# Optimization experiments

Hardware: AMD Instinct MI355X
Metric: run time of the kernel (lower is better)

Reference implementation:

```python
import jax, jax.numpy as jnp
import numpy as np

BOTTLENECK_DIM = 128
TOP_K = 8
SCALE = 1.0 / np.sqrt(BOTTLENECK_DIM)
EPS = 1e-10


def setup_inputs() -> dict:
    key = jax.random.key(0)
    k1, k2, k3, k4 = jax.random.split(key, 4)
    query = jax.random.normal(k1, (4, 4096, 128), dtype=jnp.float32)
    keys = jax.random.normal(k2, (4096, 128), dtype=jnp.float32)
    values = jax.random.normal(k3, (4096, 1024), dtype=jnp.float32)
    reliability = jax.random.uniform(k4, (4096,), dtype=jnp.float32)
    return {"query": query, "keys": keys, "values": values, "reliability": reliability}


def reference(query, keys, values, reliability):
    # Routing: [b, s, num_slots] scores with log-reliability bias, take top-k slots.
    router_scores = jnp.einsum("bsd,nd->bsn", query, keys) + jnp.log(reliability + EPS)
    _, top_indices = jax.lax.top_k(router_scores, TOP_K)  # [b, s, k]

    # Gather per-token slot keys/values: [b, s, k, d] and [b, s, k, h]
    selected_keys = keys[top_indices]
    selected_values = values[top_indices]

    # Small-k attention over gathered slots.
    attn_scores = jnp.einsum("bsd,bskd->bsk", query, selected_keys) * SCALE
    attn_weights = jax.nn.softmax(attn_scores, axis=-1)  # [b, s, k]
    output = jnp.einsum("bsk,bskh->bsh", attn_weights, selected_values)
    return output, attn_weights
```

## Files before the change

kernel.cpp:

```cpp
#include <hip/hip_runtime.h>
#include <hip/hip_fp16.h>
#include <math.h>

#define NSLOTS 4096
#define DIM    128
#define HDIM   1024
#define NTOK   16384
#define SCALE  0.08838834764831845f
#define REPS   1e-10f

typedef __attribute__((ext_vector_type(8))) short bf16x8;
typedef __attribute__((ext_vector_type(4))) float f32x4;

typedef __attribute__((address_space(1))) const void* as1cv;
typedef __attribute__((address_space(3))) void* as3v;

__device__ __forceinline__ float pack_score(float biased, unsigned inv_idx) {
    return __uint_as_float((__float_as_uint(biased) & 0xFFFFF000u) | inv_idx);
}
#define PACK_NEG_INF __uint_as_float(0xFF7FF000u)

__device__ __forceinline__ void ins_packed(float (&r)[8], float x) {
    #pragma unroll
    for (int i = 0; i < 7; ++i) r[i] = __builtin_amdgcn_fmed3f(r[i], x, r[i + 1]);
    r[7] = fmaxf(r[7], x);
}

__device__ __forceinline__ void merge_out16(float (&r)[8], int kseg, float* outS) {
    float hv = r[7];
    #pragma unroll
    for (int rnd = 0; rnd < 16; ++rnd) {
        float bv = hv;
        bv = fmaxf(bv, __shfl_xor(bv, 16, 64));
        bv = fmaxf(bv, __shfl_xor(bv, 32, 64));
        if ((rnd >> 2) == kseg) outS[rnd] = bv;
        if (hv == bv) {
            #pragma unroll
            for (int m2 = 7; m2 > 0; --m2) r[m2] = r[m2 - 1];
            r[0] = PACK_NEG_INF;
            hv = r[7];
        }
    }
}

__device__ __forceinline__ ushort f2bf(float f) {
    unsigned u = __float_as_uint(f);
    return (ushort)((u + 0x7fffu + ((u >> 16) & 1u)) >> 16);
}
#define QB_N  524288
#define KBP_N 65536
#define LR_N  4096
#define VH_N  524288
__global__ void prep_kernel(const float* __restrict__ q, const float* __restrict__ k,
                            const float* __restrict__ rel, const float* __restrict__ v,
                            ushort* __restrict__ qb, ushort* __restrict__ kbp,
                            float* __restrict__ lr, ushort* __restrict__ vh) {
    int gid = blockIdx.x * 256 + threadIdx.x;
    if (gid < QB_N) {
        float4 vv = ((const float4*)q)[gid];
        ushort4 o; o.x = f2bf(vv.x); o.y = f2bf(vv.y); o.z = f2bf(vv.z); o.w = f2bf(vv.w);
        ((ushort4*)qb)[gid] = o;
    } else if (gid < QB_N + KBP_N) {
        int C = gid - QB_N;
        int l = C & 63, kc = (C >> 6) & 3, t16 = C >> 8;
        int slot = t16 * 16 + (l & 15);
        int doff = kc * 32 + (l >> 4) * 8;
        const float4* src = (const float4*)(k + (size_t)slot * DIM + doff);
        float4 v0 = src[0], v1 = src[1];
        union { ushort u[8]; uint4 v; } o;
        o.u[0] = f2bf(v0.x); o.u[1] = f2bf(v0.y); o.u[2] = f2bf(v0.z); o.u[3] = f2bf(v0.w);
        o.u[4] = f2bf(v1.x); o.u[5] = f2bf(v1.y); o.u[6] = f2bf(v1.z); o.u[7] = f2bf(v1.w);
        ((uint4*)kbp)[C] = o.v;
    } else if (gid < QB_N + KBP_N + LR_N) {
        int g = gid - QB_N - KBP_N;
        lr[g] = logf(rel[g] + REPS);
    } else if (gid < QB_N + KBP_N + LR_N + VH_N) {
        int g = gid - QB_N - KBP_N - LR_N;
        const float4* src = (const float4*)v + (size_t)g * 2;
        float4 a = src[0], b = src[1];
        union { _Float16 h[8]; uint4 u; } o;
        o.h[0] = (_Float16)a.x; o.h[1] = (_Float16)a.y;
        o.h[2] = (_Float16)a.z; o.h[3] = (_Float16)a.w;
        o.h[4] = (_Float16)b.x; o.h[5] = (_Float16)b.y;
        o.h[6] = (_Float16)b.z; o.h[7] = (_Float16)b.w;
        ((uint4*)vh)[g] = o.u;
    }
}

__launch_bounds__(256, 4)
__global__ void route_kernel(const ushort* __restrict__ qb,
                             const ushort* __restrict__ kbp,
                             const float*  __restrict__ lr,
                             int* __restrict__ cand) {
    __shared__ ushort ktile[4][2][4 * 512];
    __shared__ float  qS[32][4][16];
    const int tid  = threadIdx.x;
    const int lane = tid & 63;
    const int w    = tid >> 6;
    const int m    = lane & 15;
    const int kseg = lane >> 4;
    const int tokbase = blockIdx.x * 32;

    bf16x8 bF0[4], bF1[4];
    const ushort* q0 = qb + (size_t)(tokbase + m) * DIM + kseg * 8;
    const ushort* q1 = qb + (size_t)(tokbase + 16 + m) * DIM + kseg * 8;
    #pragma unroll
    for (int kc = 0; kc < 4; ++kc) {
        bF0[kc] = *(const bf16x8*)(q0 + kc * 32);
        bF1[kc] = *(const bf16x8*)(q1 + kc * 32);
    }

    float R0[8], R1[8];
    #pragma unroll
    for (int i = 0; i < 8; ++i) { R0[i] = PACK_NEG_INF; R1[i] = PACK_NEG_INF; }

    auto issue = [&](int t, int buf) {
        const ushort* gt = kbp + ((size_t)((w * 64 + t) * 256 + lane)) * 8;
        ushort* lb = &ktile[w][buf][0];
        #pragma unroll
        for (int i = 0; i < 4; ++i) {
            __builtin_amdgcn_global_load_lds((as1cv)(gt + i * 512),
                                             (as3v)(lb + i * 512 + lane * 8), 16, 0, 0);
        }
    };

    issue(0, 0);
    issue(1, 1);

    for (int t = 0; t < 64; ++t) {
        const int cur = t & 1;
        if (t < 63) {
            asm volatile("s_waitcnt vmcnt(4)" ::: "memory");
        } else {
            asm volatile("s_waitcnt vmcnt(0)" ::: "memory");
        }
        const ushort* kt = &ktile[w][cur][0];
        bf16x8 aF[4];
        #pragma unroll
        for (int kc = 0; kc < 4; ++kc)
            aF[kc] = *(const bf16x8*)(kt + kc * 512 + lane * 8);
        asm volatile("s_waitcnt lgkmcnt(0)" ::: "memory");
        if (t < 62) issue(t + 2, cur);

        f32x4 acc0 = {0.f, 0.f, 0.f, 0.f};
        f32x4 acc1 = {0.f, 0.f, 0.f, 0.f};
        #pragma unroll
        for (int kc = 0; kc < 4; ++kc) {
            acc0 = __builtin_amdgcn_mfma_f32_16x16x32_bf16(aF[kc], bF0[kc], acc0, 0, 0, 0);
            acc1 = __builtin_amdgcn_mfma_f32_16x16x32_bf16(aF[kc], bF1[kc], acc1, 0, 0, 0);
        }
        const int base = w * 1024 + t * 16;
        float4 lrv = ((const float4*)lr)[(base >> 2) + kseg];
        unsigned invb = 4095u - (unsigned)(base + kseg * 4);
        ins_packed(R0, pack_score(acc0[0] + lrv.x, invb));
        ins_packed(R0, pack_score(acc0[1] + lrv.y, invb - 1));
        ins_packed(R0, pack_score(acc0[2] + lrv.z, invb - 2));
        ins_packed(R0, pack_score(acc0[3] + lrv.w, invb - 3));
        ins_packed(R1, pack_score(acc1[0] + lrv.x, invb));
        ins_packed(R1, pack_score(acc1[1] + lrv.y, invb - 1));
        ins_packed(R1, pack_score(acc1[2] + lrv.z, invb - 2));
        ins_packed(R1, pack_score(acc1[3] + lrv.w, invb - 3));
    }

    merge_out16(R0, kseg, &qS[m][w][0]);
    merge_out16(R1, kseg, &qS[m + 16][w][0]);
    __syncthreads();

    if (tid < 32) {
        const int token = tokbase + tid;
        int p[4] = {0, 0, 0, 0};
        #pragma unroll
        for (int c = 0; c < 16; ++c) {
            float bv = -INFINITY; int bq = 0;
            #pragma unroll
            for (int j = 0; j < 4; ++j) {
                float v = (p[j] < 16) ? qS[tid][j][p[j]] : -INFINITY;
                if (v > bv) { bv = v; bq = j; }
            }
            cand[(size_t)token * 16 + c] = 4095 - (int)(__float_as_uint(bv) & 0xFFFu);
            ++p[bq];
        }
    }
}

__device__ __forceinline__ float2 h2f2(unsigned u) {
    return __half22float2(*reinterpret_cast<const __half2*>(&u));
}
__launch_bounds__(512, 4)
__global__ void rescue_gather_kernel(const float* __restrict__ query,
                                     const float* __restrict__ keys,
                                     const float* __restrict__ lr,
                                     const int*   __restrict__ cand,
                                     const ushort* __restrict__ vh,
                                     float* __restrict__ out,
                                     float* __restrict__ wout) {
    __shared__ float4 pbuf[4][4][64];
    const int tid  = threadIdx.x;
    const int wv   = tid >> 6;
    const int tw   = wv >> 1;
    const int par  = wv & 1;
    const int lane = tid & 63;
    const int token = blockIdx.x * 4 + tw;
    const int c  = lane >> 2;
    const int qp = lane & 3;

    int ci = cand[(size_t)token * 16 + c];
    const float4* q4 = (const float4*)(query + (size_t)token * DIM) + qp * 8;
    const float4* k4 = (const float4*)(keys  + (size_t)ci    * DIM) + qp * 8;
    float sum = 0.f;
    #pragma unroll
    for (int i = 0; i < 8; ++i) {
        float4 a = q4[i], b = k4[i];
        sum = fmaf(a.x, b.x, sum); sum = fmaf(a.y, b.y, sum);
        sum = fmaf(a.z, b.z, sum); sum = fmaf(a.w, b.w, sum);
    }
    sum += __shfl_xor(sum, 1, 4);
    sum += __shfl_xor(sum, 2, 4);
    float raw = sum;
    float s   = sum + lr[ci];

    #pragma unroll
    for (int k = 2; k <= 16; k <<= 1) {
        #pragma unroll
        for (int j = k >> 1; j >= 1; j >>= 1) {
            int off = j << 2;
            float s2 = __shfl_xor(s,   off, 64);
            float r2 = __shfl_xor(raw, off, 64);
            int   i2 = __shfl_xor(ci,  off, 64);
            bool mineFirst = (s > s2) || (s == s2 && ci < i2);
            bool lower = (c & j) == 0;
            bool asc   = (c & k) == 0;
            bool keep  = (lower == asc) ? mineFirst : !mineFirst;
            if (!keep) { s = s2; raw = r2; ci = i2; }
        }
    }
    float rsel[8]; int isel[8];
    #pragma unroll
    for (int r = 0; r < 8; ++r) {
        rsel[r] = __shfl(raw, r * 4, 64);
        isel[r] = __shfl(ci,  r * 4, 64);
    }

    float mx = -INFINITY;
    #pragma unroll
    for (int k = 0; k < 8; ++k) { rsel[k] *= SCALE; mx = fmaxf(mx, rsel[k]); }
    float e[8]; float ssum = 0.f;
    #pragma unroll
    for (int k = 0; k < 8; ++k) { e[k] = expf(rsel[k] - mx); ssum += e[k]; }
    float inv = 1.0f / ssum;
    float wk[8];
    #pragma unroll
    for (int k = 0; k < 8; ++k) wk[k] = e[k] * inv;

    if (par == 0 && lane == 0) {
        #pragma unroll
        for (int k = 0; k < 8; ++k) wout[(size_t)token * 8 + k] = wk[k];
    }

    float oA[8], oB[8];
    #pragma unroll
    for (int i = 0; i < 8; ++i) { oA[i] = 0.f; oB[i] = 0.f; }
    #pragma unroll
    for (int kk = 0; kk < 4; ++kk) {
        const int k = par * 4 + kk;
        const uint4* vr = (const uint4*)vh + (size_t)isel[k] * 128;
        float wkk = wk[k];
        uint4 va = vr[lane];
        uint4 vb = vr[lane + 64];
        float2 f;
        f = h2f2(va.x); oA[0] = fmaf(wkk, f.x, oA[0]); oA[1] = fmaf(wkk, f.y, oA[1]);
        f = h2f2(va.y); oA[2] = fmaf(wkk, f.x, oA[2]); oA[3] = fmaf(wkk, f.y, oA[3]);
        f = h2f2(va.z); oA[4] = fmaf(wkk, f.x, oA[4]); oA[5] = fmaf(wkk, f.y, oA[5]);
        f = h2f2(va.w); oA[6] = fmaf(wkk, f.x, oA[6]); oA[7] = fmaf(wkk, f.y, oA[7]);
        f = h2f2(vb.x); oB[0] = fmaf(wkk, f.x, oB[0]); oB[1] = fmaf(wkk, f.y, oB[1]);
        f = h2f2(vb.y); oB[2] = fmaf(wkk, f.x, oB[2]); oB[3] = fmaf(wkk, f.y, oB[3]);
        f = h2f2(vb.z); oB[4] = fmaf(wkk, f.x, oB[4]); oB[5] = fmaf(wkk, f.y, oB[5]);
        f = h2f2(vb.w); oB[6] = fmaf(wkk, f.x, oB[6]); oB[7] = fmaf(wkk, f.y, oB[7]);
    }

    if (par) {
        pbuf[tw][0][lane] = make_float4(oA[0], oA[1], oA[2], oA[3]);
        pbuf[tw][1][lane] = make_float4(oA[4], oA[5], oA[6], oA[7]);
        pbuf[tw][2][lane] = make_float4(oB[0], oB[1], oB[2], oB[3]);
        pbuf[tw][3][lane] = make_float4(oB[4], oB[5], oB[6], oB[7]);
    }
    __syncthreads();
    if (!par) {
        float4 pA0 = pbuf[tw][0][lane], pA1 = pbuf[tw][1][lane];
        float4 pB0 = pbuf[tw][2][lane], pB1 = pbuf[tw][3][lane];
        float4* orow = (float4*)(out + (size_t)token * HDIM);
        orow[lane * 2]           = make_float4(oA[0] + pA0.x, oA[1] + pA0.y,
                                               oA[2] + pA0.z, oA[3] + pA0.w);
        orow[lane * 2 + 1]       = make_float4(oA[4] + pA1.x, oA[5] + pA1.y,
                                               oA[6] + pA1.z, oA[7] + pA1.w);
        orow[128 + lane * 2]     = make_float4(oB[0] + pB0.x, oB[1] + pB0.y,
                                               oB[2] + pB0.z, oB[3] + pB0.w);
        orow[128 + lane * 2 + 1] = make_float4(oB[4] + pB1.x, oB[5] + pB1.y,
                                               oB[6] + pB1.z, oB[7] + pB1.w);
    }
}

extern "C" void kernel_launch(void* const* d_in, const int* in_sizes, int n_in,
                              void* d_out, int out_size, void* d_ws, size_t ws_size,
                              hipStream_t stream) {
    const float* query  = (const float*)d_in[0];
    const float* keys   = (const float*)d_in[1];
    const float* values = (const float*)d_in[2];
    const float* rel    = (const float*)d_in[3];

    float* out  = (float*)d_out;
    float* wout = out + (size_t)NTOK * HDIM;

    char* ws = (char*)d_ws;
    float*  lr   = (float*)ws;   ws += 4096 * 4;
    ushort* qb   = (ushort*)ws;  ws += (size_t)NTOK * DIM * 2;
    ushort* kbp  = (ushort*)ws;  ws += (size_t)NSLOTS * DIM * 2;
    int*    cand = (int*)ws;     ws += (size_t)NTOK * 16 * 4;
    ushort* vh   = (ushort*)ws;

    int prep_grid = (QB_N + KBP_N + LR_N + VH_N) / 256;
    hipLaunchKernelGGL(prep_kernel, dim3(prep_grid), dim3(256), 0, stream,
                       query, keys, rel, values, qb, kbp, lr, vh);
    hipLaunchKernelGGL(route_kernel, dim3(NTOK / 32), dim3(256), 0, stream,
                       qb, kbp, lr, cand);
    hipLaunchKernelGGL(rescue_gather_kernel, dim3(NTOK / 4), dim3(512), 0, stream,
                       query, keys, lr, cand, vh, out, wout);
}
```

Before: 221.2 us.

## Split routing over slot halves and gather by value-column halves

```diff
diff --git a/kernel.cpp b/kernel.cpp
--- a/kernel.cpp
+++ b/kernel.cpp
@@ -76,6 +76,8 @@
         lr[g] = logf(rel[g] + REPS);
     } else if (gid < QB_N + KBP_N + LR_N + VH_N) {
         int g = gid - QB_N - KBP_N - LR_N;
+        int slot = g >> 7;
+        int d0   = (g & 127) * 8;
         const float4* src = (const float4*)v + (size_t)g * 2;
         float4 a = src[0], b = src[1];
         union { _Float16 h[8]; uint4 u; } o;
@@ -83,7 +85,10 @@
         o.h[2] = (_Float16)a.z; o.h[3] = (_Float16)a.w;
         o.h[4] = (_Float16)b.x; o.h[5] = (_Float16)b.y;
         o.h[6] = (_Float16)b.z; o.h[7] = (_Float16)b.w;
-        ((uint4*)vh)[g] = o.u;
+        size_t didx = (d0 < 512)
+            ? ((size_t)slot * 64 + (d0 >> 3))
+            : ((size_t)4096 * 64 + (size_t)slot * 64 + ((d0 - 512) >> 3));
+        ((uint4*)vh)[didx] = o.u;
     }
 }
 
@@ -91,15 +96,18 @@
 __global__ void route_kernel(const ushort* __restrict__ qb,
                              const ushort* __restrict__ kbp,
                              const float*  __restrict__ lr,
-                             int* __restrict__ cand) {
-    __shared__ ushort ktile[4][2][4 * 512];
+                             float* __restrict__ cpool) {
+    __shared__ ushort ktile[4][2][2048];
     __shared__ float  qS[32][4][16];
     const int tid  = threadIdx.x;
     const int lane = tid & 63;
     const int w    = tid >> 6;
     const int m    = lane & 15;
     const int kseg = lane >> 4;
-    const int tokbase = blockIdx.x * 32;
+    const int tg   = blockIdx.x >> 1;
+    const int half = blockIdx.x & 1;
+    const int tokbase = tg * 32;
+    const int tilebase = half * 128 + w * 32;
 
     bf16x8 bF0[4], bF1[4];
     const ushort* q0 = qb + (size_t)(tokbase + m) * DIM + kseg * 8;
@@ -115,7 +123,7 @@
     for (int i = 0; i < 8; ++i) { R0[i] = PACK_NEG_INF; R1[i] = PACK_NEG_INF; }
 
     auto issue = [&](int t, int buf) {
-        const ushort* gt = kbp + ((size_t)((w * 64 + t) * 256 + lane)) * 8;
+        const ushort* gt = kbp + ((size_t)((tilebase + t) * 256 + lane)) * 8;
         ushort* lb = &ktile[w][buf][0];
         #pragma unroll
         for (int i = 0; i < 4; ++i) {
@@ -127,9 +135,9 @@
     issue(0, 0);
     issue(1, 1);
 
-    for (int t = 0; t < 64; ++t) {
+    for (int t = 0; t < 32; ++t) {
         const int cur = t & 1;
-        if (t < 63) {
+        if (t < 31) {
             asm volatile("s_waitcnt vmcnt(4)" ::: "memory");
         } else {
             asm volatile("s_waitcnt vmcnt(0)" ::: "memory");
@@ -140,7 +148,7 @@
         for (int kc = 0; kc < 4; ++kc)
             aF[kc] = *(const bf16x8*)(kt + kc * 512 + lane * 8);
         asm volatile("s_waitcnt lgkmcnt(0)" ::: "memory");
-        if (t < 62) issue(t + 2, cur);
+        if (t < 30) issue(t + 2, cur);
 
         f32x4 acc0 = {0.f, 0.f, 0.f, 0.f};
         f32x4 acc1 = {0.f, 0.f, 0.f, 0.f};
@@ -149,7 +157,7 @@
             acc0 = __builtin_amdgcn_mfma_f32_16x16x32_bf16(aF[kc], bF0[kc], acc0, 0, 0, 0);
             acc1 = __builtin_amdgcn_mfma_f32_16x16x32_bf16(aF[kc], bF1[kc], acc1, 0, 0, 0);
         }
-        const int base = w * 1024 + t * 16;
+        const int base = half * 2048 + w * 512 + t * 16;
         float4 lrv = ((const float4*)lr)[(base >> 2) + kseg];
         unsigned invb = 4095u - (unsigned)(base + kseg * 4);
         ins_packed(R0, pack_score(acc0[0] + lrv.x, invb));
@@ -177,7 +185,7 @@
                 float v = (p[j] < 16) ? qS[tid][j][p[j]] : -INFINITY;
                 if (v > bv) { bv = v; bq = j; }
             }
-            cand[(size_t)token * 16 + c] = 4095 - (int)(__float_as_uint(bv) & 0xFFFu);
+            cpool[(size_t)token * 32 + half * 16 + c] = bv;
             ++p[bq];
         }
     }
@@ -186,44 +194,47 @@
 __device__ __forceinline__ float2 h2f2(unsigned u) {
     return __half22float2(*reinterpret_cast<const __half2*>(&u));
 }
-__launch_bounds__(512, 4)
+__launch_bounds__(256)
 __global__ void rescue_gather_kernel(const float* __restrict__ query,
                                      const float* __restrict__ keys,
                                      const float* __restrict__ lr,
-                                     const int*   __restrict__ cand,
+                                     const float* __restrict__ cpool,
                                      const ushort* __restrict__ vh,
                                      float* __restrict__ out,
                                      float* __restrict__ wout) {
-    __shared__ float4 pbuf[4][4][64];
     const int tid  = threadIdx.x;
     const int wv   = tid >> 6;
-    const int tw   = wv >> 1;
-    const int par  = wv & 1;
     const int lane = tid & 63;
-    const int token = blockIdx.x * 4 + tw;
-    const int c  = lane >> 2;
-    const int qp = lane & 3;
-
-    int ci = cand[(size_t)token * 16 + c];
-    const float4* q4 = (const float4*)(query + (size_t)token * DIM) + qp * 8;
-    const float4* k4 = (const float4*)(keys  + (size_t)ci    * DIM) + qp * 8;
+    const int b    = blockIdx.x;
+    const int x    = b & 7;
+    const int dhalf = x >> 2;
+    const int tg   = (b >> 3) * 4 + (x & 3);
+    const int token = tg * 4 + wv;
+    const int c  = lane >> 1;
+    const int h  = lane & 1;
+
+    float pv = cpool[(size_t)token * 32 + c];
+    int ci = 4095 - (int)(__float_as_uint(pv) & 0xFFFu);
+
+    const f32x4* q4 = (const f32x4*)(query + (size_t)token * DIM + h * 64);
+    const float4* k4 = (const float4*)(keys + (size_t)ci * DIM + h * 64);
     float sum = 0.f;
     #pragma unroll
-    for (int i = 0; i < 8; ++i) {
-        float4 a = q4[i], b = k4[i];
-        sum = fmaf(a.x, b.x, sum); sum = fmaf(a.y, b.y, sum);
-        sum = fmaf(a.z, b.z, sum); sum = fmaf(a.w, b.w, sum);
-    }
-    sum += __shfl_xor(sum, 1, 4);
-    sum += __shfl_xor(sum, 2, 4);
+    for (int i = 0; i < 16; ++i) {
+        f32x4  a = __builtin_nontemporal_load(q4 + i);
+        float4 bb = k4[i];
+        sum = fmaf(a.x, bb.x, sum); sum = fmaf(a.y, bb.y, sum);
+        sum = fmaf(a.z, bb.z, sum); sum = fmaf(a.w, bb.w, sum);
+    }
+    sum += __shfl_xor(sum, 1, 2);
     float raw = sum;
     float s   = sum + lr[ci];
 
     #pragma unroll
-    for (int k = 2; k <= 16; k <<= 1) {
+    for (int k = 2; k <= 32; k <<= 1) {
         #pragma unroll
         for (int j = k >> 1; j >= 1; j >>= 1) {
-            int off = j << 2;
+            int off = j << 1;
             float s2 = __shfl_xor(s,   off, 64);
             float r2 = __shfl_xor(raw, off, 64);
             int   i2 = __shfl_xor(ci,  off, 64);
@@ -237,8 +248,8 @@
     float rsel[8]; int isel[8];
     #pragma unroll
     for (int r = 0; r < 8; ++r) {
-        rsel[r] = __shfl(raw, r * 4, 64);
-        isel[r] = __shfl(ci,  r * 4, 64);
+        rsel[r] = __shfl(raw, r * 2, 64);
+        isel[r] = __shfl(ci,  r * 2, 64);
     }
 
     float mx = -INFINITY;
@@ -252,52 +263,30 @@
     #pragma unroll
     for (int k = 0; k < 8; ++k) wk[k] = e[k] * inv;
 
-    if (par == 0 && lane == 0) {
+    if (dhalf == 0 && lane == 0) {
         #pragma unroll
         for (int k = 0; k < 8; ++k) wout[(size_t)token * 8 + k] = wk[k];
     }
 
-    float oA[8], oB[8];
-    #pragma unroll
-    for (int i = 0; i < 8; ++i) { oA[i] = 0.f; oB[i] = 0.f; }
-    #pragma unroll
-    for (int kk = 0; kk < 4; ++kk) {
-        const int k = par * 4 + kk;
-        const uint4* vr = (const uint4*)vh + (size_t)isel[k] * 128;
+    const uint4* vbase = (const uint4*)vh + (size_t)dhalf * 4096 * 64;
+    float o[8];
+    #pragma unroll
+    for (int i = 0; i < 8; ++i) o[i] = 0.f;
+    #pragma unroll
+    for (int k = 0; k < 8; ++k) {
+        const uint4 va = vbase[(size_t)isel[k] * 64 + lane];
         float wkk = wk[k];
-        uint4 va = vr[lane];
-        uint4 vb = vr[lane + 64];
         float2 f;
-        f = h2f2(va.x); oA[0] = fmaf(wkk, f.x, oA[0]); oA[1] = fmaf(wkk, f.y, oA[1]);
-        f = h2f2(va.y); oA[2] = fmaf(wkk, f.x, oA[2]); oA[3] = fmaf(wkk, f.y, oA[3]);
-        f = h2f2(va.z); oA[4] = fmaf(wkk, f.x, oA[4]); oA[5] = fmaf(wkk, f.y, oA[5]);
-        f = h2f2(va.w); oA[6] = fmaf(wkk, f.x, oA[6]); oA[7] = fmaf(wkk, f.y, oA[7]);
-        f = h2f2(vb.x); oB[0] = fmaf(wkk, f.x, oB[0]); oB[1] = fmaf(wkk, f.y, oB[1]);
-        f = h2f2(vb.y); oB[2] = fmaf(wkk, f.x, oB[2]); oB[3] = fmaf(wkk, f.y, oB[3]);
-        f = h2f2(vb.z); oB[4] = fmaf(wkk, f.x, oB[4]); oB[5] = fmaf(wkk, f.y, oB[5]);
-        f = h2f2(vb.w); oB[6] = fmaf(wkk, f.x, oB[6]); oB[7] = fmaf(wkk, f.y, oB[7]);
-    }
-
-    if (par) {
-        pbuf[tw][0][lane] = make_float4(oA[0], oA[1], oA[2], oA[3]);
-        pbuf[tw][1][lane] = make_float4(oA[4], oA[5], oA[6], oA[7]);
-        pbuf[tw][2][lane] = make_float4(oB[0], oB[1], oB[2], oB[3]);
-        pbuf[tw][3][lane] = make_float4(oB[4], oB[5], oB[6], oB[7]);
-    }
-    __syncthreads();
-    if (!par) {
-        float4 pA0 = pbuf[tw][0][lane], pA1 = pbuf[tw][1][lane];
-        float4 pB0 = pbuf[tw][2][lane], pB1 = pbuf[tw][3][lane];
-        float4* orow = (float4*)(out + (size_t)token * HDIM);
-        orow[lane * 2]           = make_float4(oA[0] + pA0.x, oA[1] + pA0.y,
-                                               oA[2] + pA0.z, oA[3] + pA0.w);
-        orow[lane * 2 + 1]       = make_float4(oA[4] + pA1.x, oA[5] + pA1.y,
-                                               oA[6] + pA1.z, oA[7] + pA1.w);
-        orow[128 + lane * 2]     = make_float4(oB[0] + pB0.x, oB[1] + pB0.y,
-                                               oB[2] + pB0.z, oB[3] + pB0.w);
-        orow[128 + lane * 2 + 1] = make_float4(oB[4] + pB1.x, oB[5] + pB1.y,
-                                               oB[6] + pB1.z, oB[7] + pB1.w);
-    }
+        f = h2f2(va.x); o[0] = fmaf(wkk, f.x, o[0]); o[1] = fmaf(wkk, f.y, o[1]);
+        f = h2f2(va.y); o[2] = fmaf(wkk, f.x, o[2]); o[3] = fmaf(wkk, f.y, o[3]);
+        f = h2f2(va.z); o[4] = fmaf(wkk, f.x, o[4]); o[5] = fmaf(wkk, f.y, o[5]);
+        f = h2f2(va.w); o[6] = fmaf(wkk, f.x, o[6]); o[7] = fmaf(wkk, f.y, o[7]);
+    }
+    f32x4* orow = (f32x4*)(out + (size_t)token * HDIM + dhalf * 512 + lane * 8);
+    f32x4 s0 = {o[0], o[1], o[2], o[3]};
+    f32x4 s1 = {o[4], o[5], o[6], o[7]};
+    __builtin_nontemporal_store(s0, orow);
+    __builtin_nontemporal_store(s1, orow + 1);
 }
 
 extern "C" void kernel_launch(void* const* d_in, const int* in_sizes, int n_in,
@@ -312,17 +301,17 @@
     float* wout = out + (size_t)NTOK * HDIM;
 
     char* ws = (char*)d_ws;
-    float*  lr   = (float*)ws;   ws += 4096 * 4;
-    ushort* qb   = (ushort*)ws;  ws += (size_t)NTOK * DIM * 2;
-    ushort* kbp  = (ushort*)ws;  ws += (size_t)NSLOTS * DIM * 2;
-    int*    cand = (int*)ws;     ws += (size_t)NTOK * 16 * 4;
-    ushort* vh   = (ushort*)ws;
+    float*  lr    = (float*)ws;   ws += 4096 * 4;
+    ushort* qb    = (ushort*)ws;  ws += (size_t)NTOK * DIM * 2;
+    ushort* kbp   = (ushort*)ws;  ws += (size_t)NSLOTS * DIM * 2;
+    float*  cpool = (float*)ws;   ws += (size_t)NTOK * 32 * 4;
+    ushort* vh    = (ushort*)ws;
 
     int prep_grid = (QB_N + KBP_N + LR_N + VH_N) / 256;
     hipLaunchKernelGGL(prep_kernel, dim3(prep_grid), dim3(256), 0, stream,
                        query, keys, rel, values, qb, kbp, lr, vh);
-    hipLaunchKernelGGL(route_kernel, dim3(NTOK / 32), dim3(256), 0, stream,
-                       qb, kbp, lr, cand);
-    hipLaunchKernelGGL(rescue_gather_kernel, dim3(NTOK / 4), dim3(512), 0, stream,
-                       query, keys, lr, cand, vh, out, wout);
-}
+    hipLaunchKernelGGL(route_kernel, dim3(NTOK / 16), dim3(256), 0, stream,
+                       qb, kbp, lr, cpool);
+    hipLaunchKernelGGL(rescue_gather_kernel, dim3(NTOK / 2), dim3(256), 0, stream,
+                       query, keys, lr, cpool, vh, out, wout);
+}
```

Result: slower. 284.9 us (+28.8%).
